# Kernel tuning notes

Measured on AMD Instinct MI355X. Metric: run time of the kernel, lower is better.

## Reference

```python
import jax, jax.numpy as jnp
import numpy as np

N = 100000      # nodes
E = 1600000     # edges (before self-loops)
F_IN = 512      # input features
H = 8           # heads layer 1
D = 8           # per-head dim layer 1
C = 40          # classes (layer 2 out, heads=1)
NEG_SLOPE = 0.2 # PyG GATConv default negative_slope


def setup_inputs() -> dict:
    key = jax.random.key(0)
    ks = jax.random.split(key, 10)
    x = jax.random.normal(ks[0], (N, F_IN), jnp.float32)
    edge_index = jax.random.randint(ks[1], (2, E), 0, N, dtype=jnp.int32)
    W1 = jax.random.normal(ks[2], (F_IN, H * D), jnp.float32) / np.float32(np.sqrt(F_IN))
    att_src1 = jax.random.normal(ks[3], (H, D), jnp.float32) / np.float32(np.sqrt(D))
    att_dst1 = jax.random.normal(ks[4], (H, D), jnp.float32) / np.float32(np.sqrt(D))
    b1 = jnp.zeros((H * D,), jnp.float32)
    W2 = jax.random.normal(ks[5], (H * D, C), jnp.float32) / np.float32(np.sqrt(H * D))
    att_src2 = jax.random.normal(ks[6], (1, C), jnp.float32) / np.float32(np.sqrt(C))
    att_dst2 = jax.random.normal(ks[7], (1, C), jnp.float32) / np.float32(np.sqrt(C))
    b2 = jnp.zeros((C,), jnp.float32)
    return {"x": x, "edge_index": edge_index, "W1": W1, "att_src1": att_src1,
            "att_dst1": att_dst1, "b1": b1, "W2": W2, "att_src2": att_src2,
            "att_dst2": att_dst2, "b2": b2}


def _gat_layer(x, src, dst, W, a_src, a_dst, heads, dim):
    # Dense projection, then per-head attention logits.
    h = (x @ W).reshape(-1, heads, dim)            # [N, H, D]
    alpha_s = jnp.einsum('nhd,hd->nh', h, a_src)   # [N, H]
    alpha_d = jnp.einsum('nhd,hd->nh', h, a_dst)
    e = jax.nn.leaky_relu(alpha_s[src] + alpha_d[dst], NEG_SLOPE)  # [E, H]
    # Segment softmax over edges grouped by destination node.
    emax = jax.ops.segment_max(e, dst, num_segments=N)
    emax = jnp.where(jnp.isfinite(emax), emax, 0.0)
    ee = jnp.exp(e - emax[dst])
    denom = jax.ops.segment_sum(ee, dst, num_segments=N)
    alpha = ee / (denom[dst] + 1e-16)              # [E, H]
    # Scatter-aggregate weighted neighbor features.
    msg = h[src] * alpha[:, :, None]               # [E, H, D]
    return jax.ops.segment_sum(msg, dst, num_segments=N)  # [N, H, D]


def reference(x, edge_index, W1, att_src1, att_dst1, b1, W2, att_src2, att_dst2, b2):
    # PyG GATConv adds self-loops by default.
    loops = jnp.arange(N, dtype=edge_index.dtype)
    src = jnp.concatenate([edge_index[0], loops])
    dst = jnp.concatenate([edge_index[1], loops])
    # Layer 1: 8 heads, concat=True, then ELU. (dropouts identity in eval mode)
    h1 = _gat_layer(x, src, dst, W1, att_src1, att_dst1, H, D).reshape(N, H * D) + b1
    h1 = jax.nn.elu(h1)
    # Layer 2: 1 head, concat=False -> mean over heads (trivial for H=1).
    h2 = _gat_layer(h1, src, dst, W2, att_src2, att_dst2, 1, C)[:, 0, :] + b2
    return jax.nn.log_softmax(h2, axis=1)
```

## Files before the change

kernel.cpp:

```cpp
#include <hip/hip_runtime.h>

#define F_IN   512
#define HD     64
#define NHEAD  8
#define NC     40
#define NEG    0.2f

typedef __attribute__((ext_vector_type(8))) short bf16x8;
typedef __attribute__((ext_vector_type(4))) float f32x4;

__device__ __forceinline__ float lrelu(float x) { return x > 0.0f ? x : NEG * x; }

__device__ __forceinline__ short f2bf(float f) {
    unsigned u = __float_as_uint(f);
    u += 0x7FFF + ((u >> 16) & 1);
    return (short)(u >> 16);
}
__device__ __forceinline__ float bf2f(short h) {
    return __uint_as_float(((unsigned)(unsigned short)h) << 16);
}
__device__ __forceinline__ float bfl(unsigned u) { return __uint_as_float(u << 16); }
__device__ __forceinline__ float bfh(unsigned u) { return __uint_as_float(u & 0xFFFF0000u); }

__global__ void zero_kernel(int* __restrict__ p, int n) {
    int i = blockIdx.x * 256 + threadIdx.x;
    if (i < n) p[i] = 0;
}

__global__ __launch_bounds__(256) void scanA_kernel(const int* __restrict__ deg,
                                                    int* __restrict__ incl,
                                                    int* __restrict__ bsum, int Nn) {
    __shared__ int wsum[4];
    int t = threadIdx.x, b = blockIdx.x;
    int base = b * 1024 + t * 4;
    int v0 = (base + 0) < Nn ? deg[base + 0] : 0;
    int v1 = (base + 1) < Nn ? deg[base + 1] : 0;
    int v2 = (base + 2) < Nn ? deg[base + 2] : 0;
    int v3 = (base + 3) < Nn ? deg[base + 3] : 0;
    int p0 = v0, p1 = p0 + v1, p2 = p1 + v2, p3 = p2 + v3;
    int lane = t & 63, w = t >> 6;
    int sc = p3;
    for (int off = 1; off < 64; off <<= 1) {
        int u = __shfl_up(sc, off);
        if (lane >= off) sc += u;
    }
    if (lane == 63) wsum[w] = sc;
    __syncthreads();
    int woff = 0;
#pragma unroll
    for (int i = 0; i < 4; ++i) if (i < w) woff += wsum[i];
    int excl = woff + sc - p3;
    if (base + 0 < Nn) incl[base + 0] = excl + p0;
    if (base + 1 < Nn) incl[base + 1] = excl + p1;
    if (base + 2 < Nn) incl[base + 2] = excl + p2;
    if (base + 3 < Nn) incl[base + 3] = excl + p3;
    if (t == 0) bsum[b] = wsum[0] + wsum[1] + wsum[2] + wsum[3];
}

__global__ void scanB_kernel(int* __restrict__ bsum, int nb) {
    int lane = threadIdx.x;
    int a = lane < nb ? bsum[lane] : 0;
    int c = (lane + 64) < nb ? bsum[lane + 64] : 0;
    int sa = a, sc2 = c;
    for (int off = 1; off < 64; off <<= 1) {
        int u = __shfl_up(sa, off);  if (lane >= off) sa += u;
        int u2 = __shfl_up(sc2, off); if (lane >= off) sc2 += u2;
    }
    int totA = __shfl(sa, 63);
    int ea = sa - a;
    int ec = totA + sc2 - c;
    if (lane < nb) bsum[lane] = ea;
    if (lane + 64 < nb) bsum[lane + 64] = ec;
}

__global__ void scanC_kernel(const int* __restrict__ incl, const int* __restrict__ bsum,
                             int* __restrict__ rp, int Nn) {
    int i = blockIdx.x * 256 + threadIdx.x;
    if (i == 0) rp[0] = 0;
    if (i < Nn) rp[i + 1] = incl[i] + bsum[i >> 10];
}

__global__ void scatter_kernel(const int* __restrict__ src, const int* __restrict__ dst,
                               const int* __restrict__ pos, const int* __restrict__ rp,
                               int* __restrict__ col, int E) {
    int e = blockIdx.x * 256 + threadIdx.x;
    if (e < E) {
        int d = dst[e];
        col[rp[d] + pos[e]] = src[e];
    }
}

#define G1_BM 64
__global__ __launch_bounds__(256) void g1c_kernel(const float* __restrict__ X,
                                                  const float* __restrict__ W,
                                                  const float* __restrict__ att_s,
                                                  const float* __restrict__ att_d,
                                                  unsigned short* __restrict__ Hp,
                                                  float* __restrict__ as1,
                                                  float* __restrict__ ad1,
                                                  const int* __restrict__ dst,
                                                  int* __restrict__ deg,
                                                  int* __restrict__ pos,
                                                  int Nn, int E, int nG1) {
    __shared__ short Bh[2][4][HD][8];
    __shared__ short Bl[2][4][HD][8];
    int tid = threadIdx.x;

    if ((int)blockIdx.x >= nG1) {
        int e = ((int)blockIdx.x - nG1) * 256 + tid;
        if (e < E) pos[e] = atomicAdd(&deg[dst[e]], 1);
        return;
    }

    int wid = tid >> 6, lane = tid & 63;
    int lrow = lane & 15, kgrp = lane >> 4;
    int row0 = blockIdx.x * G1_BM;
    int rowA = row0 + wid * 16 + lrow;

    int sc = tid & 63, ks = tid >> 6;

    float ats[4], atd[4];
#pragma unroll
    for (int fc = 0; fc < 4; ++fc) { ats[fc] = att_s[fc * 16 + lrow]; atd[fc] = att_d[fc * 16 + lrow]; }

    f32x4 acc[4];
#pragma unroll
    for (int fc = 0; fc < 4; ++fc) acc[fc] = (f32x4){0.f, 0.f, 0.f, 0.f};

    bool valid = rowA < Nn;
    const float* xrow = X + (size_t)rowA * F_IN + kgrp * 8;

    float4 a_cur[2][2], a_nxt[2][2];
#pragma unroll
    for (int kb = 0; kb < 2; ++kb) {
        if (valid) {
            a_cur[kb][0] = *reinterpret_cast<const float4*>(xrow + kb * 32);
            a_cur[kb][1] = *reinterpret_cast<const float4*>(xrow + kb * 32 + 4);
        } else {
            a_cur[kb][0] = a_cur[kb][1] = make_float4(0.f, 0.f, 0.f, 0.f);
        }
    }

    for (int it = 0; it < F_IN / 64; ++it) {
        int k0 = it * 64;
        float wreg[16];
#pragma unroll
        for (int j = 0; j < 16; ++j)
            wreg[j] = W[(size_t)(k0 + ks * 16 + j) * HD + sc];
        if (it + 1 < F_IN / 64) {
#pragma unroll
            for (int kb = 0; kb < 2; ++kb) {
                if (valid) {
                    const float* p = xrow + (k0 + 64) + kb * 32;
                    a_nxt[kb][0] = *reinterpret_cast<const float4*>(p);
                    a_nxt[kb][1] = *reinterpret_cast<const float4*>(p + 4);
                } else {
                    a_nxt[kb][0] = a_nxt[kb][1] = make_float4(0.f, 0.f, 0.f, 0.f);
                }
            }
        }
        bf16x8 af[2];
#pragma unroll
        for (int kb = 0; kb < 2; ++kb) {
            float fs[8] = {a_cur[kb][0].x, a_cur[kb][0].y, a_cur[kb][0].z, a_cur[kb][0].w,
                           a_cur[kb][1].x, a_cur[kb][1].y, a_cur[kb][1].z, a_cur[kb][1].w};
#pragma unroll
            for (int j = 0; j < 8; ++j) af[kb][j] = f2bf(fs[j]);
        }
        __syncthreads();
#pragma unroll
        for (int half = 0; half < 2; ++half) {
            bf16x8 vh, vl;
#pragma unroll
            for (int j = 0; j < 8; ++j) {
                float wv = wreg[half * 8 + j];
                short hh = f2bf(wv);
                vh[j] = hh;
                vl[j] = f2bf(wv - bf2f(hh));
            }
            int kk = ks * 2 + half;
            *reinterpret_cast<bf16x8*>(&Bh[kk >> 2][kk & 3][sc][0]) = vh;
            *reinterpret_cast<bf16x8*>(&Bl[kk >> 2][kk & 3][sc][0]) = vl;
        }
        __syncthreads();
#pragma unroll
        for (int kb = 0; kb < 2; ++kb) {
#pragma unroll
            for (int fc = 0; fc < 4; ++fc) {
                bf16x8 bh = *reinterpret_cast<const bf16x8*>(&Bh[kb][kgrp][fc * 16 + lrow][0]);
                bf16x8 bl = *reinterpret_cast<const bf16x8*>(&Bl[kb][kgrp][fc * 16 + lrow][0]);
                acc[fc] = __builtin_amdgcn_mfma_f32_16x16x32_bf16(af[kb], bh, acc[fc], 0, 0, 0);
                acc[fc] = __builtin_amdgcn_mfma_f32_16x16x32_bf16(af[kb], bl, acc[fc], 0, 0, 0);
            }
        }
        if (it + 1 < F_IN / 64) {
#pragma unroll
            for (int kb = 0; kb < 2; ++kb) {
                a_cur[kb][0] = a_nxt[kb][0];
                a_cur[kb][1] = a_nxt[kb][1];
            }
        }
    }

#pragma unroll
    for (int r = 0; r < 4; ++r) {
        int gr = row0 + wid * 16 + kgrp * 4 + r;
        float hv[4], sp[4], dp[4];
#pragma unroll
        for (int fc = 0; fc < 4; ++fc) {
            hv[fc] = acc[fc][r];
            sp[fc] = hv[fc] * ats[fc];
            dp[fc] = hv[fc] * atd[fc];
        }
#pragma unroll
        for (int mask = 1; mask <= 4; mask <<= 1) {
#pragma unroll
            for (int fc = 0; fc < 4; ++fc) {
                sp[fc] += __shfl_xor(sp[fc], mask);
                dp[fc] += __shfl_xor(dp[fc], mask);
            }
        }
        if (gr < Nn) {
#pragma unroll
            for (int fc = 0; fc < 4; ++fc)
                Hp[(size_t)gr * HD + fc * 16 + lrow] = (unsigned short)f2bf(hv[fc]);
            if ((lane & 7) == 0) {
                int hh = lrow >> 3;
#pragma unroll
                for (int fc = 0; fc < 4; ++fc) {
                    as1[gr * NHEAD + fc * 2 + hh] = sp[fc];
                    ad1[gr * NHEAD + fc * 2 + hh] = dp[fc];
                }
            }
        }
    }
}

__global__ __launch_bounds__(256) void agg1_kernel(const unsigned short* __restrict__ Hp,
                                                   const float* __restrict__ as1,
                                                   const float* __restrict__ ad1,
                                                   const int* __restrict__ col,
                                                   const int* __restrict__ rp,
                                                   const float* __restrict__ b1,
                                                   float* __restrict__ h1, int Nn) {
    int n = blockIdx.x * 4 + (threadIdx.x >> 6);
    int lane = threadIdx.x & 63;
    if (n >= Nn) return;
    int slot = lane >> 3, j = lane & 7;
    int beg = rp[n], end = rp[n + 1];
    float adv1 = ad1[n * NHEAD + j];
    float acc[8] = {0, 0, 0, 0, 0, 0, 0, 0};
    float dw = 0.f;
    for (int t = beg + slot; t < end; t += 8) {
        int s = col[t];
        float w = __expf(lrelu(as1[s * NHEAD + j] + adv1));
        dw += w;
        uint4 u = *reinterpret_cast<const uint4*>(&Hp[(size_t)s * HD + j * 8]);
        acc[0] += w * bfl(u.x); acc[1] += w * bfh(u.x);
        acc[2] += w * bfl(u.y); acc[3] += w * bfh(u.y);
        acc[4] += w * bfl(u.z); acc[5] += w * bfh(u.z);
        acc[6] += w * bfl(u.w); acc[7] += w * bfh(u.w);
    }
#pragma unroll
    for (int mask = 8; mask < 64; mask <<= 1) {
#pragma unroll
        for (int i = 0; i < 8; ++i) acc[i] += __shfl_xor(acc[i], mask);
        dw += __shfl_xor(dw, mask);
    }
    float w = __expf(lrelu(as1[n * NHEAD + j] + adv1));
    uint4 u = *reinterpret_cast<const uint4*>(&Hp[(size_t)n * HD + j * 8]);
    acc[0] += w * bfl(u.x); acc[1] += w * bfh(u.x);
    acc[2] += w * bfl(u.y); acc[3] += w * bfh(u.y);
    acc[4] += w * bfl(u.z); acc[5] += w * bfh(u.z);
    acc[6] += w * bfl(u.w); acc[7] += w * bfh(u.w);
    dw += w;
    float invd = 1.0f / (dw + 1e-16f);
    float4 b0 = *reinterpret_cast<const float4*>(&b1[j * 8]);
    float4 b4 = *reinterpret_cast<const float4*>(&b1[j * 8 + 4]);
    float bb[8] = {b0.x, b0.y, b0.z, b0.w, b4.x, b4.y, b4.z, b4.w};
#pragma unroll
    for (int i = 0; i < 8; ++i) {
        float v = acc[i] * invd + bb[i];
        acc[i] = v > 0.0f ? v : __expf(v) - 1.0f;
    }
    if (slot == 0) {
        float4 o0 = make_float4(acc[0], acc[1], acc[2], acc[3]);
        float4 o1 = make_float4(acc[4], acc[5], acc[6], acc[7]);
        *reinterpret_cast<float4*>(&h1[(size_t)n * HD + j * 8]) = o0;
        *reinterpret_cast<float4*>(&h1[(size_t)n * HD + j * 8 + 4]) = o1;
    }
}

#define G2R 64
__global__ __launch_bounds__(256) void gemm2_kernel(const float* __restrict__ H1,
                                                    const float* __restrict__ W2,
                                                    const float* __restrict__ asw,
                                                    const float* __restrict__ adw,
                                                    unsigned int* __restrict__ h2p,
                                                    float* __restrict__ as2,
                                                    float* __restrict__ ad2, int Nn) {
    __shared__ float Hs[G2R][HD + 1];
    __shared__ float W2s[HD][NC];
    __shared__ float asv[NC], adv[NC];
    int tid = threadIdx.x;
    for (int i = tid; i < HD * NC; i += 256) W2s[i / NC][i % NC] = W2[i];
    if (tid < NC) { asv[tid] = asw[tid]; adv[tid] = adw[tid]; }
    int row0 = blockIdx.x * G2R;
#pragma unroll
    for (int i = 0; i < 4; ++i) {
        int linear = i * 1024 + tid * 4;
        int r = linear >> 6, c = linear & 63;
        int gr = row0 + r;
        float4 v = make_float4(0.f, 0.f, 0.f, 0.f);
        if (gr < Nn) v = *reinterpret_cast<const float4*>(&H1[(size_t)gr * HD + c]);
        Hs[r][c + 0] = v.x; Hs[r][c + 1] = v.y; Hs[r][c + 2] = v.z; Hs[r][c + 3] = v.w;
    }
    __syncthreads();
    int row = tid >> 2, cg = tid & 3;
    int gr = row0 + row;
    float acc[10];
#pragma unroll
    for (int jj = 0; jj < 10; ++jj) acc[jj] = 0.0f;
    for (int k = 0; k < HD; ++k) {
        float a = Hs[row][k];
#pragma unroll
        for (int jj = 0; jj < 10; ++jj) acc[jj] += a * W2s[k][cg * 10 + jj];
    }
    float sa = 0.0f, da = 0.0f;
#pragma unroll
    for (int jj = 0; jj < 10; ++jj) {
        sa += acc[jj] * asv[cg * 10 + jj];
        da += acc[jj] * adv[cg * 10 + jj];
    }
    sa += __shfl_xor(sa, 1); sa += __shfl_xor(sa, 2);
    da += __shfl_xor(da, 1); da += __shfl_xor(da, 2);
    if (gr < Nn) {
        if (cg == 0) { as2[gr] = sa; ad2[gr] = da; }
#pragma unroll
        for (int jj = 0; jj < 5; ++jj) {
            unsigned int u = ((unsigned int)(unsigned short)f2bf(acc[2 * jj + 1]) << 16) |
                             (unsigned short)f2bf(acc[2 * jj]);
            h2p[(size_t)gr * 20 + cg * 5 + jj] = u;
        }
    }
}

__global__ __launch_bounds__(256) void agg2_kernel(const unsigned int* __restrict__ h2p,
                                                   const float* __restrict__ as2,
                                                   const float* __restrict__ ad2,
                                                   const int* __restrict__ col,
                                                   const int* __restrict__ rp,
                                                   const float* __restrict__ b2,
                                                   float* __restrict__ out, int Nn) {
    int n = blockIdx.x * 4 + (threadIdx.x >> 6);
    int lane = threadIdx.x & 63;
    if (n >= Nn) return;
    int slot = lane >> 4, l16 = lane & 15;
    bool act = l16 < 10;
    int beg = rp[n], end = rp[n + 1];
    float adv = ad2[n];
    float4 acc = make_float4(0.f, 0.f, 0.f, 0.f);
    float dw = 0.f;
    for (int t = beg + slot; t < end; t += 4) {
        int s = col[t];
        float w = __expf(lrelu(as2[s] + adv));
        dw += w;
        if (act) {
            uint2 u = *reinterpret_cast<const uint2*>(&h2p[(size_t)s * 20 + l16 * 2]);
            acc.x += w * bfl(u.x); acc.y += w * bfh(u.x);
            acc.z += w * bfl(u.y); acc.w += w * bfh(u.y);
        }
    }
#pragma unroll
    for (int mask = 16; mask < 64; mask <<= 1) {
        acc.x += __shfl_xor(acc.x, mask);
        acc.y += __shfl_xor(acc.y, mask);
        acc.z += __shfl_xor(acc.z, mask);
        acc.w += __shfl_xor(acc.w, mask);
        dw    += __shfl_xor(dw, mask);
    }
    float w = __expf(lrelu(as2[n] + adv));
    dw += w;
    float invd = 1.0f / (dw + 1e-16f);
    if (act) {
        uint2 u = *reinterpret_cast<const uint2*>(&h2p[(size_t)n * 20 + l16 * 2]);
        float4 bb = *reinterpret_cast<const float4*>(&b2[l16 * 4]);
        acc.x = (acc.x + w * bfl(u.x)) * invd + bb.x;
        acc.y = (acc.y + w * bfh(u.x)) * invd + bb.y;
        acc.z = (acc.z + w * bfl(u.y)) * invd + bb.z;
        acc.w = (acc.w + w * bfh(u.y)) * invd + bb.w;
    }
    float mloc = act ? fmaxf(fmaxf(acc.x, acc.y), fmaxf(acc.z, acc.w)) : -INFINITY;
#pragma unroll
    for (int mask = 1; mask < 16; mask <<= 1) mloc = fmaxf(mloc, __shfl_xor(mloc, mask));
    float s4 = act ? (__expf(acc.x - mloc) + __expf(acc.y - mloc) +
                      __expf(acc.z - mloc) + __expf(acc.w - mloc)) : 0.0f;
#pragma unroll
    for (int mask = 1; mask < 16; mask <<= 1) s4 += __shfl_xor(s4, mask);
    float lse = mloc + __logf(s4);
    if (slot == 0 && act) {
        float4 o = make_float4(acc.x - lse, acc.y - lse, acc.z - lse, acc.w - lse);
        *reinterpret_cast<float4*>(&out[(size_t)n * NC + l16 * 4]) = o;
    }
}

extern "C" void kernel_launch(void* const* d_in, const int* in_sizes, int n_in,
                              void* d_out, int out_size, void* d_ws, size_t ws_size,
                              hipStream_t stream) {
    const float* x    = (const float*)d_in[0];
    const int*   ei   = (const int*)d_in[1];
    const float* W1   = (const float*)d_in[2];
    const float* as1w = (const float*)d_in[3];
    const float* ad1w = (const float*)d_in[4];
    const float* b1   = (const float*)d_in[5];
    const float* W2   = (const float*)d_in[6];
    const float* as2w = (const float*)d_in[7];
    const float* ad2w = (const float*)d_in[8];
    const float* b2   = (const float*)d_in[9];
    float* out = (float*)d_out;

    int Nn = in_sizes[0] / F_IN;
    int E  = in_sizes[1] / 2;
    const int* srcv = ei;
    const int* dstv = ei + E;

    char* ws = (char*)d_ws;
    size_t off = 0;
    auto alloc = [&](size_t bytes) { size_t cur = off; off += (bytes + 255) & ~255ULL; return cur; };
    unsigned short* Hp = (unsigned short*)(ws + alloc((size_t)Nn * HD * 2));
    float* h1   = (float*)(ws + alloc((size_t)Nn * HD * 4));
    float* as1v = (float*)(ws + alloc((size_t)Nn * NHEAD * 4));
    float* ad1v = (float*)(ws + alloc((size_t)Nn * NHEAD * 4));
    unsigned int* h2p = (unsigned int*)(ws + alloc((size_t)Nn * 20 * 4));
    float* as2v = (float*)(ws + alloc((size_t)Nn * 4));
    float* ad2v = (float*)(ws + alloc((size_t)Nn * 4));
    int* deg  = (int*)(ws + alloc((size_t)Nn * 4));
    int* incl = (int*)(ws + alloc((size_t)Nn * 4));
    int* rp   = (int*)(ws + alloc((size_t)(Nn + 1) * 4));
    int* pos  = (int*)(ws + alloc((size_t)E * 4));
    int* col  = (int*)(ws + alloc((size_t)E * 4));
    int* bsum = (int*)(ws + alloc(256 * 4));

    int nb   = (Nn + 1023) / 1024;
    int nG1  = (Nn + G1_BM - 1) / G1_BM;
    int nCNT = (E + 255) / 256;

    zero_kernel<<<(Nn + 255) / 256, 256, 0, stream>>>(deg, Nn);
    g1c_kernel<<<nG1 + nCNT, 256, 0, stream>>>(x, W1, as1w, ad1w, Hp, as1v, ad1v,
                                               dstv, deg, pos, Nn, E, nG1);
    scanA_kernel<<<nb, 256, 0, stream>>>(deg, incl, bsum, Nn);
    scanB_kernel<<<1, 64, 0, stream>>>(bsum, nb);
    scanC_kernel<<<(Nn + 255) / 256, 256, 0, stream>>>(incl, bsum, rp, Nn);
    scatter_kernel<<<(E + 255) / 256, 256, 0, stream>>>(srcv, dstv, pos, rp, col, E);

    agg1_kernel<<<(Nn + 3) / 4, 256, 0, stream>>>(Hp, as1v, ad1v, col, rp, b1, h1, Nn);
    gemm2_kernel<<<(Nn + G2R - 1) / G2R, 256, 0, stream>>>(h1, W2, as2w, ad2w, h2p, as2v, ad2v, Nn);
    agg2_kernel<<<(Nn + 3) / 4, 256, 0, stream>>>(h2p, as2v, ad2v, col, rp, b2, out, Nn);
}
```

Before: 317.3 us.

## Pre-split W1 into bf16 hi/lo once and read MFMA fragments from global

Adds a small kernel that converts W1 into bf16 high and low parts once, stored in an MFMA-fragment-friendly layout. The projection GEMM now loads B fragments straight from global memory (L2-resident) instead of each block redoing the split and staging it through shared memory behind two barriers. The K loop is rebuilt to step 32 at a time with a one-step X prefetch. This removes redundant conversion work and block-level syncs, at the cost of one extra launch and more global/L2 load traffic per MFMA.

```diff
diff --git a/kernel.cpp b/kernel.cpp
--- a/kernel.cpp
+++ b/kernel.cpp
@@ -90,9 +90,22 @@
     }
 }
 
+__global__ void wsplit_kernel(const float* __restrict__ W, short* __restrict__ Whp,
+                              short* __restrict__ Wlp) {
+    int t = blockIdx.x * 256 + threadIdx.x;
+    if (t >= F_IN * HD) return;
+    int k = t >> 6, c = t & 63;
+    float wv = W[t];
+    short hh = f2bf(wv);
+    int idx = (((k >> 3) * 64 + c) << 3) + (k & 7);
+    Whp[idx] = hh;
+    Wlp[idx] = f2bf(wv - bf2f(hh));
+}
+
 #define G1_BM 64
 __global__ __launch_bounds__(256) void g1c_kernel(const float* __restrict__ X,
-                                                  const float* __restrict__ W,
+                                                  const short* __restrict__ Whp,
+                                                  const short* __restrict__ Wlp,
                                                   const float* __restrict__ att_s,
                                                   const float* __restrict__ att_d,
                                                   unsigned short* __restrict__ Hp,
@@ -102,8 +115,6 @@
                                                   int* __restrict__ deg,
                                                   int* __restrict__ pos,
                                                   int Nn, int E, int nG1) {
-    __shared__ short Bh[2][4][HD][8];
-    __shared__ short Bl[2][4][HD][8];
     int tid = threadIdx.x;
 
     if ((int)blockIdx.x >= nG1) {
@@ -117,8 +128,6 @@
     int row0 = blockIdx.x * G1_BM;
     int rowA = row0 + wid * 16 + lrow;
 
-    int sc = tid & 63, ks = tid >> 6;
-
     float ats[4], atd[4];
 #pragma unroll
     for (int fc = 0; fc < 4; ++fc) { ats[fc] = att_s[fc * 16 + lrow]; atd[fc] = att_d[fc * 16 + lrow]; }
@@ -129,77 +138,46 @@
 
     bool valid = rowA < Nn;
     const float* xrow = X + (size_t)rowA * F_IN + kgrp * 8;
-
-    float4 a_cur[2][2], a_nxt[2][2];
-#pragma unroll
-    for (int kb = 0; kb < 2; ++kb) {
-        if (valid) {
-            a_cur[kb][0] = *reinterpret_cast<const float4*>(xrow + kb * 32);
-            a_cur[kb][1] = *reinterpret_cast<const float4*>(xrow + kb * 32 + 4);
-        } else {
-            a_cur[kb][0] = a_cur[kb][1] = make_float4(0.f, 0.f, 0.f, 0.f);
-        }
-    }
-
-    for (int it = 0; it < F_IN / 64; ++it) {
-        int k0 = it * 64;
-        float wreg[16];
-#pragma unroll
-        for (int j = 0; j < 16; ++j)
-            wreg[j] = W[(size_t)(k0 + ks * 16 + j) * HD + sc];
-        if (it + 1 < F_IN / 64) {
-#pragma unroll
-            for (int kb = 0; kb < 2; ++kb) {
-                if (valid) {
-                    const float* p = xrow + (k0 + 64) + kb * 32;
-                    a_nxt[kb][0] = *reinterpret_cast<const float4*>(p);
-                    a_nxt[kb][1] = *reinterpret_cast<const float4*>(p + 4);
-                } else {
-                    a_nxt[kb][0] = a_nxt[kb][1] = make_float4(0.f, 0.f, 0.f, 0.f);
-                }
+    const bf16x8* WhV = reinterpret_cast<const bf16x8*>(Whp);
+    const bf16x8* WlV = reinterpret_cast<const bf16x8*>(Wlp);
+
+    float4 a_cur[2], a_nxt[2];
+    if (valid) {
+        a_cur[0] = *reinterpret_cast<const float4*>(xrow);
+        a_cur[1] = *reinterpret_cast<const float4*>(xrow + 4);
+    } else {
+        a_cur[0] = a_cur[1] = make_float4(0.f, 0.f, 0.f, 0.f);
+    }
+
+#pragma unroll 2
+    for (int it = 0; it < F_IN / 32; ++it) {
+        if (it + 1 < F_IN / 32) {
+            if (valid) {
+                const float* p = xrow + (it + 1) * 32;
+                a_nxt[0] = *reinterpret_cast<const float4*>(p);
+                a_nxt[1] = *reinterpret_cast<const float4*>(p + 4);
+            } else {
+                a_nxt[0] = a_nxt[1] = make_float4(0.f, 0.f, 0.f, 0.f);
             }
         }
-        bf16x8 af[2];
-#pragma unroll
-        for (int kb = 0; kb < 2; ++kb) {
-            float fs[8] = {a_cur[kb][0].x, a_cur[kb][0].y, a_cur[kb][0].z, a_cur[kb][0].w,
-                           a_cur[kb][1].x, a_cur[kb][1].y, a_cur[kb][1].z, a_cur[kb][1].w};
-#pragma unroll
-            for (int j = 0; j < 8; ++j) af[kb][j] = f2bf(fs[j]);
-        }
-        __syncthreads();
-#pragma unroll
-        for (int half = 0; half < 2; ++half) {
-            bf16x8 vh, vl;
-#pragma unroll
-            for (int j = 0; j < 8; ++j) {
-                float wv = wreg[half * 8 + j];
-                short hh = f2bf(wv);
-                vh[j] = hh;
-                vl[j] = f2bf(wv - bf2f(hh));
-            }
-            int kk = ks * 2 + half;
-            *reinterpret_cast<bf16x8*>(&Bh[kk >> 2][kk & 3][sc][0]) = vh;
-            *reinterpret_cast<bf16x8*>(&Bl[kk >> 2][kk & 3][sc][0]) = vl;
-        }
-        __syncthreads();
-#pragma unroll
-        for (int kb = 0; kb < 2; ++kb) {
-#pragma unroll
-            for (int fc = 0; fc < 4; ++fc) {
-                bf16x8 bh = *reinterpret_cast<const bf16x8*>(&Bh[kb][kgrp][fc * 16 + lrow][0]);
-                bf16x8 bl = *reinterpret_cast<const bf16x8*>(&Bl[kb][kgrp][fc * 16 + lrow][0]);
-                acc[fc] = __builtin_amdgcn_mfma_f32_16x16x32_bf16(af[kb], bh, acc[fc], 0, 0, 0);
-                acc[fc] = __builtin_amdgcn_mfma_f32_16x16x32_bf16(af[kb], bl, acc[fc], 0, 0, 0);
-            }
-        }
-        if (it + 1 < F_IN / 64) {
-#pragma unroll
-            for (int kb = 0; kb < 2; ++kb) {
-                a_cur[kb][0] = a_nxt[kb][0];
-                a_cur[kb][1] = a_nxt[kb][1];
-            }
-        }
+        bf16x8 af;
+        {
+            float fs[8] = {a_cur[0].x, a_cur[0].y, a_cur[0].z, a_cur[0].w,
+                           a_cur[1].x, a_cur[1].y, a_cur[1].z, a_cur[1].w};
+#pragma unroll
+            for (int j = 0; j < 8; ++j) af[j] = f2bf(fs[j]);
+        }
+        const bf16x8* bhp = WhV + (size_t)(it * 4 + kgrp) * 64;
+        const bf16x8* blp = WlV + (size_t)(it * 4 + kgrp) * 64;
+#pragma unroll
+        for (int fc = 0; fc < 4; ++fc) {
+            bf16x8 bh = bhp[fc * 16 + lrow];
+            bf16x8 bl = blp[fc * 16 + lrow];
+            acc[fc] = __builtin_amdgcn_mfma_f32_16x16x32_bf16(af, bh, acc[fc], 0, 0, 0);
+            acc[fc] = __builtin_amdgcn_mfma_f32_16x16x32_bf16(af, bl, acc[fc], 0, 0, 0);
+        }
+        a_cur[0] = a_nxt[0];
+        a_cur[1] = a_nxt[1];
     }
 
 #pragma unroll
@@ -440,13 +418,16 @@
     int* pos  = (int*)(ws + alloc((size_t)E * 4));
     int* col  = (int*)(ws + alloc((size_t)E * 4));
     int* bsum = (int*)(ws + alloc(256 * 4));
+    short* Whp = (short*)(ws + alloc((size_t)F_IN * HD * 2));
+    short* Wlp = (short*)(ws + alloc((size_t)F_IN * HD * 2));
 
     int nb   = (Nn + 1023) / 1024;
     int nG1  = (Nn + G1_BM - 1) / G1_BM;
     int nCNT = (E + 255) / 256;
 
     zero_kernel<<<(Nn + 255) / 256, 256, 0, stream>>>(deg, Nn);
-    g1c_kernel<<<nG1 + nCNT, 256, 0, stream>>>(x, W1, as1w, ad1w, Hp, as1v, ad1v,
+    wsplit_kernel<<<(F_IN * HD + 255) / 256, 256, 0, stream>>>(W1, Whp, Wlp);
+    g1c_kernel<<<nG1 + nCNT, 256, 0, stream>>>(x, Whp, Wlp, as1w, ad1w, Hp, as1v, ad1v,
                                                dstv, deg, pos, Nn, E, nG1);
     scanA_kernel<<<nb, 256, 0, stream>>>(deg, incl, bsum, Nn);
     scanB_kernel<<<1, 64, 0, stream>>>(bsum, nb);
```

New measurement: 351.4 us. 10.8% more time.
